# Performance work log

Hardware: AMD Instinct MI355X
Metric: run time of the kernel (lower is better)

The kernel has to match this reference:

```python
import jax, jax.numpy as jnp
import numpy as np


def setup_inputs() -> dict:
    key = jax.random.key(0)
    k1, k2, k3, k4 = jax.random.split(key, 4)
    B, E, R, D = 1024, 8192, 16, 128
    head = jax.random.randint(k1, (B,), 0, E)
    tail = jax.random.randint(k2, (B,), 0, E)
    entity_embeddings = jax.random.normal(k3, (E, D), dtype=jnp.float32)
    rule_embeddings = jax.random.normal(k4, (R, D), dtype=jnp.float32)
    return {
        "head": head,
        "tail": tail,
        "query_relation": 3,
        "depth": 1,
        "entity_embeddings": entity_embeddings,
        "rule_embeddings": rule_embeddings,
    }


def reference(head, tail, query_relation, depth, entity_embeddings, rule_embeddings):
    # NeuralTheoremProver.prove at depth == 1 (deepest runnable config):
    #   score[b] = sum_r mean_z  s1[r,b,z] * s2[b,z]
    #   s1[r,b,z] = -|| e[head_b] + rule_r - e[z] ||_2       (base_case of prove #1)
    #   s2[b,z]   = -|| e[z] + rule_q - e[tail_b] ||_2       (base_case of prove #2)
    # Squared L2 is expanded via dot products so we never materialize [R,B,E,D].
    E_tab = entity_embeddings                      # [E, D]
    h = E_tab[head]                                # [B, D]
    t = E_tab[tail]                                # [B, D]
    hh = jnp.sum(h * h, axis=-1)                   # [B]
    tt = jnp.sum(t * t, axis=-1)                   # [B]
    zz = jnp.sum(E_tab * E_tab, axis=-1)           # [E]
    rr = jnp.sum(rule_embeddings * rule_embeddings, axis=-1)  # [R]

    hr = h @ rule_embeddings.T                     # [B, R]
    hz = h @ E_tab.T                               # [B, E]
    rz = rule_embeddings @ E_tab.T                 # [R, E]

    # ||h + r - z||^2 = hh + rr + zz + 2 h.r - 2 h.z - 2 r.z   -> [R, B, E]
    sq1 = (hh[None, :, None] + rr[:, None, None] + zz[None, None, :]
           + 2.0 * hr.T[:, :, None] - 2.0 * hz[None, :, :] - 2.0 * rz[:, None, :])
    S1 = -jnp.sum(jnp.sqrt(jnp.maximum(sq1, 0.0)), axis=0)     # [B, E] = sum_r s1

    q = rule_embeddings[query_relation]            # [D]
    qq = jnp.sum(q * q)
    zq = E_tab @ q                                 # [E]
    zt = t @ E_tab.T                               # [B, E]
    qt = t @ q                                     # [B]
    # ||z + q - t||^2 = zz + qq + tt + 2 z.q - 2 z.t - 2 q.t   -> [B, E]
    sq2 = zz[None, :] + qq + tt[:, None] + 2.0 * zq[None, :] - 2.0 * zt - 2.0 * qt[:, None]
    s2 = -jnp.sqrt(jnp.maximum(sq2, 0.0))          # [B, E]

    return jnp.mean(S1 * s2, axis=1)               # [B]
```

## Files before the change

kernel.cpp:

```cpp
#include <hip/hip_runtime.h>


typedef __attribute__((ext_vector_type(8))) short short8;
typedef __attribute__((ext_vector_type(4))) float f32x4;

__device__ inline unsigned short f2bf(float f) {
  unsigned int u = __float_as_uint(f);
  u += 0x7fffu + ((u >> 16) & 1u);
  return (unsigned short)(u >> 16);
}

__global__ __launch_bounds__(256) void ntp_pre(
    const float* __restrict__ Etab, const float* __restrict__ rules,
    const int* __restrict__ head, const int* __restrict__ tail,
    const int* __restrict__ qrelp, unsigned short* __restrict__ Ebf,
    unsigned short* __restrict__ Hbf, unsigned short* __restrict__ Tbf,
    float* __restrict__ Gz, float* __restrict__ G2, float* __restrict__ C1,
    float* __restrict__ C2, float* __restrict__ out, int nEB) {
  const int tid = threadIdx.x;
  const int gl = tid >> 4;
  const int r  = tid & 15;
  const int qrel = qrelp[0];
  const float* rp = rules + (size_t)r * 128;

  if ((int)blockIdx.x < nEB) {
    const int z = blockIdx.x * 16 + gl;
    const float* ez = Etab + (size_t)z * 128;
    float rz = 0.f, zz = 0.f, rr = 0.f;
#pragma unroll
    for (int k = 0; k < 128; k += 4) {
      f32x4 ev = *reinterpret_cast<const f32x4*>(ez + k);
      f32x4 rv = *reinterpret_cast<const f32x4*>(rp + k);
#pragma unroll
      for (int j = 0; j < 4; ++j) {
        rz += ev[j] * rv[j];
        zz += ev[j] * ev[j];
        rr += rv[j] * rv[j];
      }
    }
    Gz[(size_t)z * 16 + r] = zz - 2.f * rz;
    if (r == qrel) G2[z] = zz + 2.f * rz + rr;
    const float* src = ez + r * 8;
    short8 o;
#pragma unroll
    for (int j = 0; j < 8; ++j) o[j] = (short)f2bf(src[j]);
    *reinterpret_cast<short8*>(Ebf + (size_t)z * 128 + r * 8) = o;
  } else {
    const int b = (blockIdx.x - nEB) * 16 + gl;
    const int hi = head[b], ti = tail[b];
    const float* hp = Etab + (size_t)hi * 128;
    const float* tp = Etab + (size_t)ti * 128;
    float hr = 0.f, tq = 0.f, hh = 0.f, tt = 0.f, rr = 0.f;
#pragma unroll
    for (int k = 0; k < 128; k += 4) {
      f32x4 hv = *reinterpret_cast<const f32x4*>(hp + k);
      f32x4 tv = *reinterpret_cast<const f32x4*>(tp + k);
      f32x4 rv = *reinterpret_cast<const f32x4*>(rp + k);
#pragma unroll
      for (int j = 0; j < 4; ++j) {
        hr += hv[j] * rv[j];
        tq += tv[j] * rv[j];
        hh += hv[j] * hv[j];
        tt += tv[j] * tv[j];
        rr += rv[j] * rv[j];
      }
    }
    C1[(size_t)b * 16 + r] = hh + rr + 2.f * hr;
    if (r == qrel) C2[b] = tt - 2.f * tq;
    if (r == 0) out[b] = 0.f;
    short8 oh, ot;
    const float* hsrc = hp + r * 8;
    const float* tsrc = tp + r * 8;
#pragma unroll
    for (int j = 0; j < 8; ++j) {
      oh[j] = (short)f2bf(hsrc[j]);
      ot[j] = (short)f2bf(tsrc[j]);
    }
    *reinterpret_cast<short8*>(Hbf + (size_t)b * 128 + r * 8) = oh;
    *reinterpret_cast<short8*>(Tbf + (size_t)b * 128 + r * 8) = ot;
  }
}

__global__ __launch_bounds__(256, 2) void ntp_main(
    const unsigned short* __restrict__ Ebf, const unsigned short* __restrict__ Hbf,
    const unsigned short* __restrict__ Tbf, const float* __restrict__ Gz,
    const float* __restrict__ G2, const float* __restrict__ C1,
    const float* __restrict__ C2, float* __restrict__ out, int Ecount) {
  __shared__ __align__(16) unsigned short sEz[32][136];
  __shared__ __align__(16) float sGz[32][36];
  __shared__ __align__(16) float sG2[32];
  __shared__ __align__(16) float sC1[32][16];
  __shared__ __align__(16) float sC2[32];

  const int tid   = threadIdx.x;
  const int lane  = tid & 63, wave = tid >> 6;
  const int bhalf = wave >> 1, zhalf = wave & 1;
  const int quad  = lane >> 4, lm = lane & 15;
  const int b_base = blockIdx.x * 32;
  const int z_base = blockIdx.y * 256;

  if (tid < 128) {
    *reinterpret_cast<f32x4*>(&sC1[tid >> 2][(tid & 3) * 4]) =
        *reinterpret_cast<const f32x4*>(&C1[(size_t)(b_base + (tid >> 2)) * 16 + (tid & 3) * 4]);
  }
  if (tid < 32) sC2[tid] = C2[b_base + tid];

  short8 hfrag[4], tfrag[4];
  {
    const size_t brow = (size_t)(b_base + bhalf * 16 + lm) * 128 + quad * 8;
    const unsigned short* hp = Hbf + brow;
    const unsigned short* tp = Tbf + brow;
#pragma unroll
    for (int k4 = 0; k4 < 4; ++k4) {
      hfrag[k4] = *reinterpret_cast<const short8*>(hp + k4 * 32);
      tfrag[k4] = *reinterpret_cast<const short8*>(tp + k4 * 32);
    }
  }

  __syncthreads();
  f32x4 c1q[4][4];
  float c2v[4];
#pragma unroll
  for (int reg = 0; reg < 4; ++reg) {
    const int b_loc = bhalf * 16 + quad * 4 + reg;
#pragma unroll
    for (int i = 0; i < 4; ++i)
      c1q[reg][i] = *reinterpret_cast<const f32x4*>(&sC1[b_loc][i * 4]);
    c2v[reg] = sC2[b_loc];
  }

  const int z_loc = zhalf * 16 + lm;
  const float scale = 1.0f / (float)Ecount;
  f32x4 acc_out = {0.f, 0.f, 0.f, 0.f};

  for (int c = 0; c < 8; ++c) {
    const int z0 = z_base + c * 32;
    __syncthreads();
    {
      int u = tid;
#pragma unroll
      for (int rep = 0; rep < 2; ++rep, u += 256) {
        int row = u >> 4, col = u & 15;
        *reinterpret_cast<short8*>(&sEz[row][col * 8]) =
            *reinterpret_cast<const short8*>(Ebf + (size_t)(z0 + row) * 128 + col * 8);
      }
    }
    if (tid < 128) {
      int row = tid >> 2, col = tid & 3;
      *reinterpret_cast<f32x4*>(&sGz[row][col * 4]) =
          *reinterpret_cast<const f32x4*>(&Gz[(size_t)(z0 + row) * 16 + col * 4]);
    }
    if (tid < 32) sG2[tid] = G2[z0 + tid];
    __syncthreads();

    f32x4 acc_hz = {0.f, 0.f, 0.f, 0.f};
    f32x4 acc_zt = {0.f, 0.f, 0.f, 0.f};
#pragma unroll
    for (int k4 = 0; k4 < 4; ++k4) {
      short8 ef = *reinterpret_cast<const short8*>(&sEz[z_loc][k4 * 32 + quad * 8]);
      acc_hz = __builtin_amdgcn_mfma_f32_16x16x32_bf16(hfrag[k4], ef, acc_hz, 0, 0, 0);
      acc_zt = __builtin_amdgcn_mfma_f32_16x16x32_bf16(tfrag[k4], ef, acc_zt, 0, 0, 0);
    }

    f32x4 gr[4];
#pragma unroll
    for (int i = 0; i < 4; ++i)
      gr[i] = *reinterpret_cast<const f32x4*>(&sGz[z_loc][i * 4]);
    const float g2v = sG2[z_loc];
#pragma unroll
    for (int reg = 0; reg < 4; ++reg) {
      const float hz = acc_hz[reg], zt = acc_zt[reg];
      const float sq2 = g2v + c2v[reg] - 2.f * zt;
      const float s2 = __builtin_amdgcn_sqrtf(fmaxf(sq2, 0.f));
      const float m2hz = -2.f * hz;
      float S1 = 0.f;
#pragma unroll
      for (int i = 0; i < 4; ++i)
#pragma unroll
        for (int j = 0; j < 4; ++j) {
          const float sq1 = (c1q[reg][i][j] + gr[i][j]) + m2hz;
          S1 += __builtin_amdgcn_sqrtf(fmaxf(sq1, 0.f));
        }
      acc_out[reg] += S1 * s2;
    }
  }

#pragma unroll
  for (int reg = 0; reg < 4; ++reg) {
    float v = acc_out[reg];
    v += __shfl_xor(v, 1, 16);
    v += __shfl_xor(v, 2, 16);
    v += __shfl_xor(v, 4, 16);
    v += __shfl_xor(v, 8, 16);
    if (lm == 0)
      atomicAdd(&out[b_base + bhalf * 16 + quad * 4 + reg], v * scale);
  }
}

extern "C" void kernel_launch(void* const* d_in, const int* in_sizes, int n_in,
                              void* d_out, int out_size, void* d_ws, size_t ws_size,
                              hipStream_t stream) {
  const int* head  = (const int*)d_in[0];
  const int* tail  = (const int*)d_in[1];
  const int* qrel  = (const int*)d_in[2];
  const float* Etab  = (const float*)d_in[4];
  const float* rules = (const float*)d_in[5];
  const int B = in_sizes[0];
  const int E = in_sizes[4] / 128;
  float* out = (float*)d_out;

  char* ws = (char*)d_ws;
  unsigned short* Ebf = (unsigned short*)ws;
  unsigned short* Hbf = (unsigned short*)(ws + (size_t)E * 256);
  unsigned short* Tbf = Hbf + (size_t)B * 128;
  float* Gz = (float*)(ws + (size_t)E * 256 + (size_t)B * 512);
  float* G2 = Gz + (size_t)E * 16;
  float* C1 = G2 + E;
  float* C2 = C1 + (size_t)B * 16;

  const int nEB = E / 16;
  const int nBB = B / 16;
  ntp_pre<<<nEB + nBB, 256, 0, stream>>>(Etab, rules, head, tail, qrel, Ebf,
                                         Hbf, Tbf, Gz, G2, C1, C2, out, nEB);
  ntp_main<<<dim3(B / 32, E / 256), 256, 0, stream>>>(Ebf, Hbf, Tbf, Gz, G2, C1,
                                                      C2, out, E);
}
```

Measured before the change: 120.4 us.

## Drop LDS staging of entity tiles, read fragments from global, raise occupancy

The main kernel no longer stages Ebf, Gz and G2 tiles through shared memory with per-chunk barriers; each lane loads its MFMA fragment and Gz/G2 values directly from global memory. C1 values are re-read from LDS inside the loop instead of being held in 64 registers, and occupancy is raised to 3 blocks per SM with half the z range per block (twice as many blocks). The precompute kernel caches the rule table in LDS. This trades barrier and register pressure for more global/L2 traffic and more atomics on the output.

```diff
diff --git a/kernel.cpp b/kernel.cpp
--- a/kernel.cpp
+++ b/kernel.cpp
@@ -17,11 +17,20 @@
     unsigned short* __restrict__ Hbf, unsigned short* __restrict__ Tbf,
     float* __restrict__ Gz, float* __restrict__ G2, float* __restrict__ C1,
     float* __restrict__ C2, float* __restrict__ out, int nEB) {
+  __shared__ __align__(16) float sR[16][132];
   const int tid = threadIdx.x;
   const int gl = tid >> 4;
   const int r  = tid & 15;
   const int qrel = qrelp[0];
-  const float* rp = rules + (size_t)r * 128;
+
+#pragma unroll
+  for (int rep = 0; rep < 2; ++rep) {
+    int idx = tid + rep * 256;
+    int row = idx >> 5, colv = idx & 31;
+    *reinterpret_cast<f32x4*>(&sR[row][colv * 4]) =
+        *reinterpret_cast<const f32x4*>(rules + (size_t)row * 128 + colv * 4);
+  }
+  __syncthreads();
 
   if ((int)blockIdx.x < nEB) {
     const int z = blockIdx.x * 16 + gl;
@@ -30,7 +39,7 @@
 #pragma unroll
     for (int k = 0; k < 128; k += 4) {
       f32x4 ev = *reinterpret_cast<const f32x4*>(ez + k);
-      f32x4 rv = *reinterpret_cast<const f32x4*>(rp + k);
+      f32x4 rv = *reinterpret_cast<const f32x4*>(&sR[r][k]);
 #pragma unroll
       for (int j = 0; j < 4; ++j) {
         rz += ev[j] * rv[j];
@@ -55,7 +64,7 @@
     for (int k = 0; k < 128; k += 4) {
       f32x4 hv = *reinterpret_cast<const f32x4*>(hp + k);
       f32x4 tv = *reinterpret_cast<const f32x4*>(tp + k);
-      f32x4 rv = *reinterpret_cast<const f32x4*>(rp + k);
+      f32x4 rv = *reinterpret_cast<const f32x4*>(&sR[r][k]);
 #pragma unroll
       for (int j = 0; j < 4; ++j) {
         hr += hv[j] * rv[j];
@@ -81,29 +90,25 @@
   }
 }
 
-__global__ __launch_bounds__(256, 2) void ntp_main(
+__global__ __launch_bounds__(256, 3) void ntp_main(
     const unsigned short* __restrict__ Ebf, const unsigned short* __restrict__ Hbf,
     const unsigned short* __restrict__ Tbf, const float* __restrict__ Gz,
     const float* __restrict__ G2, const float* __restrict__ C1,
     const float* __restrict__ C2, float* __restrict__ out, int Ecount) {
-  __shared__ __align__(16) unsigned short sEz[32][136];
-  __shared__ __align__(16) float sGz[32][36];
-  __shared__ __align__(16) float sG2[32];
-  __shared__ __align__(16) float sC1[32][16];
-  __shared__ __align__(16) float sC2[32];
+  __shared__ __align__(16) float sC1[32][20];
 
   const int tid   = threadIdx.x;
   const int lane  = tid & 63, wave = tid >> 6;
   const int bhalf = wave >> 1, zhalf = wave & 1;
   const int quad  = lane >> 4, lm = lane & 15;
   const int b_base = blockIdx.x * 32;
-  const int z_base = blockIdx.y * 256;
+  const int z_base = blockIdx.y * 128;
 
   if (tid < 128) {
-    *reinterpret_cast<f32x4*>(&sC1[tid >> 2][(tid & 3) * 4]) =
-        *reinterpret_cast<const f32x4*>(&C1[(size_t)(b_base + (tid >> 2)) * 16 + (tid & 3) * 4]);
-  }
-  if (tid < 32) sC2[tid] = C2[b_base + tid];
+    int row = tid >> 2, colv = tid & 3;
+    *reinterpret_cast<f32x4*>(&sC1[row][colv * 4]) =
+        *reinterpret_cast<const f32x4*>(&C1[(size_t)(b_base + row) * 16 + colv * 4]);
+  }
 
   short8 hfrag[4], tfrag[4];
   {
@@ -117,47 +122,26 @@
     }
   }
 
+  float c2v[4];
+#pragma unroll
+  for (int reg = 0; reg < 4; ++reg)
+    c2v[reg] = C2[b_base + bhalf * 16 + quad * 4 + reg];
+
   __syncthreads();
-  f32x4 c1q[4][4];
-  float c2v[4];
-#pragma unroll
-  for (int reg = 0; reg < 4; ++reg) {
-    const int b_loc = bhalf * 16 + quad * 4 + reg;
-#pragma unroll
-    for (int i = 0; i < 4; ++i)
-      c1q[reg][i] = *reinterpret_cast<const f32x4*>(&sC1[b_loc][i * 4]);
-    c2v[reg] = sC2[b_loc];
-  }
 
   const int z_loc = zhalf * 16 + lm;
   const float scale = 1.0f / (float)Ecount;
   f32x4 acc_out = {0.f, 0.f, 0.f, 0.f};
 
-  for (int c = 0; c < 8; ++c) {
-    const int z0 = z_base + c * 32;
-    __syncthreads();
-    {
-      int u = tid;
-#pragma unroll
-      for (int rep = 0; rep < 2; ++rep, u += 256) {
-        int row = u >> 4, col = u & 15;
-        *reinterpret_cast<short8*>(&sEz[row][col * 8]) =
-            *reinterpret_cast<const short8*>(Ebf + (size_t)(z0 + row) * 128 + col * 8);
-      }
-    }
-    if (tid < 128) {
-      int row = tid >> 2, col = tid & 3;
-      *reinterpret_cast<f32x4*>(&sGz[row][col * 4]) =
-          *reinterpret_cast<const f32x4*>(&Gz[(size_t)(z0 + row) * 16 + col * 4]);
-    }
-    if (tid < 32) sG2[tid] = G2[z0 + tid];
-    __syncthreads();
-
+  for (int c = 0; c < 4; ++c) {
+    const int z = z_base + c * 32 + z_loc;
+
+    const unsigned short* ep = Ebf + (size_t)z * 128 + quad * 8;
     f32x4 acc_hz = {0.f, 0.f, 0.f, 0.f};
     f32x4 acc_zt = {0.f, 0.f, 0.f, 0.f};
 #pragma unroll
     for (int k4 = 0; k4 < 4; ++k4) {
-      short8 ef = *reinterpret_cast<const short8*>(&sEz[z_loc][k4 * 32 + quad * 8]);
+      short8 ef = *reinterpret_cast<const short8*>(ep + k4 * 32);
       acc_hz = __builtin_amdgcn_mfma_f32_16x16x32_bf16(hfrag[k4], ef, acc_hz, 0, 0, 0);
       acc_zt = __builtin_amdgcn_mfma_f32_16x16x32_bf16(tfrag[k4], ef, acc_zt, 0, 0, 0);
     }
@@ -165,22 +149,26 @@
     f32x4 gr[4];
 #pragma unroll
     for (int i = 0; i < 4; ++i)
-      gr[i] = *reinterpret_cast<const f32x4*>(&sGz[z_loc][i * 4]);
-    const float g2v = sG2[z_loc];
+      gr[i] = *reinterpret_cast<const f32x4*>(&Gz[(size_t)z * 16 + i * 4]);
+    const float g2v = G2[z];
+
 #pragma unroll
     for (int reg = 0; reg < 4; ++reg) {
+      const int b_loc = bhalf * 16 + quad * 4 + reg;
       const float hz = acc_hz[reg], zt = acc_zt[reg];
       const float sq2 = g2v + c2v[reg] - 2.f * zt;
       const float s2 = __builtin_amdgcn_sqrtf(fmaxf(sq2, 0.f));
       const float m2hz = -2.f * hz;
       float S1 = 0.f;
 #pragma unroll
-      for (int i = 0; i < 4; ++i)
+      for (int i = 0; i < 4; ++i) {
+        f32x4 c1v = *reinterpret_cast<const f32x4*>(&sC1[b_loc][i * 4]);
 #pragma unroll
         for (int j = 0; j < 4; ++j) {
-          const float sq1 = (c1q[reg][i][j] + gr[i][j]) + m2hz;
+          const float sq1 = (c1v[j] + gr[i][j]) + m2hz;
           S1 += __builtin_amdgcn_sqrtf(fmaxf(sq1, 0.f));
         }
+      }
       acc_out[reg] += S1 * s2;
     }
   }
@@ -222,6 +210,6 @@
   const int nBB = B / 16;
   ntp_pre<<<nEB + nBB, 256, 0, stream>>>(Etab, rules, head, tail, qrel, Ebf,
                                          Hbf, Tbf, Gz, G2, C1, C2, out, nEB);
-  ntp_main<<<dim3(B / 32, E / 256), 256, 0, stream>>>(Ebf, Hbf, Tbf, Gz, G2, C1,
+  ntp_main<<<dim3(B / 32, E / 128), 256, 0, stream>>>(Ebf, Hbf, Tbf, Gz, G2, C1,
                                                       C2, out, E);
 }
```

Result: faster. 113.7 us (-5.6%).
